# Kernel optimization log

Measured on AMD Instinct MI355X. Metric: run time of the kernel, lower is better.

## Reference

```python
import jax, jax.numpy as jnp
import numpy as np

S_CENTROIDS = 512
RADIUS = 0.5
NSAMPLE = 32
BN_EPS = 1e-5


def farthest_point_sample(xyz, s):
    # xyz: [B, N, 3] -> idx [B, s], deterministic start at index 0
    B, N, _ = xyz.shape

    def step(carry, _):
        dist, far = carry  # dist [B,N], far [B]
        centroid = jnp.take_along_axis(xyz, far[:, None, None], axis=1)  # [B,1,3]
        d = jnp.sum((xyz - centroid) ** 2, axis=-1)  # [B,N]
        dist = jnp.minimum(dist, d)
        nxt = jnp.argmax(dist, axis=-1).astype(jnp.int32)
        return (dist, nxt), far

    init = (jnp.full((B, N), 1e10, dtype=xyz.dtype), jnp.zeros((B,), jnp.int32))
    _, idx = jax.lax.scan(step, init, None, length=s)
    return idx.T  # [B, s]


def query_ball_point(radius, nsample, xyz, new_xyz):
    # xyz [B,N,3], new_xyz [B,S,3] -> group idx [B,S,nsample]
    B, N, _ = xyz.shape
    sqr = jnp.sum((new_xyz[:, :, None, :] - xyz[:, None, :, :]) ** 2, axis=-1)  # [B,S,N]
    gidx = jnp.where(sqr > radius * radius, N, jnp.arange(N, dtype=jnp.int32)[None, None, :])
    gidx = jnp.sort(gidx, axis=-1)[:, :, :nsample]  # closest-index-first valid ids
    first = gidx[:, :, :1]
    gidx = jnp.where(gidx == N, first, gidx)  # pad misses with first neighbor
    return gidx


def bn_relu(h, gamma, beta):
    # training-mode BatchNorm1d over (batch, length) dims of [BS, C, k]
    m = jnp.mean(h, axis=(0, 2), keepdims=True)
    v = jnp.var(h, axis=(0, 2), keepdims=True)
    hn = (h - m) / jnp.sqrt(v + BN_EPS)
    return jax.nn.relu(hn * gamma[None, :, None] + beta[None, :, None])


def setup_inputs() -> dict:
    key = jax.random.key(0)
    k1, k2, k3, k4 = jax.random.split(key, 4)
    B, N, Din, Dout = 16, 2048, 64, 128  # in_channels=2*Din=128
    x = jax.random.normal(k1, (B, Din, N), dtype=jnp.float32)
    coords = jax.random.uniform(k2, (B, N, 3), dtype=jnp.float32, minval=-1.0, maxval=1.0)
    W1 = jax.random.normal(k3, (Dout, 2 * Din), dtype=jnp.float32) * 0.05  # conv1 1x1 kernel
    W2 = jax.random.normal(k4, (Dout, Dout), dtype=jnp.float32) * 0.05    # conv2 1x1 kernel
    gamma1 = jnp.ones((Dout,), jnp.float32); beta1 = jnp.zeros((Dout,), jnp.float32)
    gamma2 = jnp.ones((Dout,), jnp.float32); beta2 = jnp.zeros((Dout,), jnp.float32)
    return {"x": x, "coords": coords, "W1": W1, "W2": W2,
            "gamma1": gamma1, "beta1": beta1, "gamma2": gamma2, "beta2": beta2}


def reference(x, coords, W1, W2, gamma1, beta1, gamma2, beta2):
    B = x.shape[0]
    feats = jnp.transpose(x, (0, 2, 1))  # [B, N, D]

    fidx = farthest_point_sample(coords, S_CENTROIDS)  # [B, s]
    bidx = jnp.arange(B)[:, None]
    new_xyz = coords[bidx, fidx]        # [B, s, 3]
    new_feat = feats[bidx, fidx]        # [B, s, D]

    gidx = query_ball_point(RADIUS, NSAMPLE, coords, new_xyz)  # [B, s, k]
    grouped = feats[jnp.arange(B)[:, None, None], gidx]        # [B, s, k, D]

    center = new_feat[:, :, None, :]
    agg = jnp.concatenate([grouped - center,
                           jnp.broadcast_to(center, grouped.shape)], axis=-1)  # [B, s, k, 2D]

    b, s, k, d = agg.shape
    h = jnp.transpose(agg, (0, 1, 3, 2)).reshape(b * s, d, k)  # [BS, 2D, k]
    h = bn_relu(jnp.einsum('bck,oc->bok', h, W1), gamma1, beta1)
    h = bn_relu(jnp.einsum('bck,oc->bok', h, W2), gamma2, beta2)
    pooled = jnp.max(h, axis=-1)                  # [BS, out]
    new_feature = jnp.transpose(pooled.reshape(b, s, -1), (0, 2, 1))  # [B, out, s]
    return new_xyz, new_feature
```

## Files before the change

kernel.cpp:

```cpp
#include <hip/hip_runtime.h>
#include <cstdint>

typedef unsigned int uint;
typedef unsigned short ushort_t;
typedef unsigned long long ull;
typedef __attribute__((ext_vector_type(8))) short bf16x8;
typedef __attribute__((ext_vector_type(4))) float f32x4;
typedef __attribute__((ext_vector_type(2))) float f32x2;

#define B_   16
#define N_   2048
#define S_   512
#define G_   8192
#define DIN  64
#define DOUT 128
#define K_   32
#define ATS  136

__device__ __forceinline__ uint bf16b(float f) {
  uint u = __float_as_uint(f);
  return (u + 0x7fffu + ((u >> 16) & 1u)) >> 16;
}
__device__ __forceinline__ float bf2f(uint b) { return __uint_as_float(b << 16); }

template<int CTRL, int RM>
__device__ __forceinline__ float dpp_fmax_step(float x) {
  float y = __uint_as_float((uint)__builtin_amdgcn_update_dpp(
      (int)__float_as_uint(x), (int)__float_as_uint(x), CTRL, RM, 0xf, true));
  return fmaxf(x, y);
}

__global__ __launch_bounds__(256) void fps_kernel(const float* __restrict__ coords,
                                                  int* __restrict__ fidx,
                                                  float* __restrict__ out_xyz) {
  int b = blockIdx.x;
  const float* cb = coords + (size_t)b * (N_ * 3);
  __shared__ float sptx[N_], spty[N_], sptz[N_];
  __shared__ ull   skey[2][4];
  __shared__ int   sfar[S_];
  int tid = threadIdx.x, lane = tid & 63, wid = tid >> 6;
  for (int j = tid; j < N_; j += 256) {
    sptx[j] = cb[3 * j]; spty[j] = cb[3 * j + 1]; sptz[j] = cb[3 * j + 2];
  }
  f32x2 px[4], py[4], pz[4], dist[4];
  int j0 = tid * 8;
#pragma unroll
  for (int p = 0; p < 4; ++p) {
    int j = j0 + 2 * p;
    px[p].x = cb[3 * j];     py[p].x = cb[3 * j + 1]; pz[p].x = cb[3 * j + 2];
    px[p].y = cb[3 * j + 3]; py[p].y = cb[3 * j + 4]; pz[p].y = cb[3 * j + 5];
    dist[p].x = 1e10f; dist[p].y = 1e10f;
  }
  float cx = cb[0], cy = cb[1], cz = cb[2];
  uint far = 0;
  __syncthreads();
  for (int s = 0; s < S_; ++s) {
    if (tid == 0) sfar[s] = (int)far;
    f32x2 c2x = {cx, cx}, c2y = {cy, cy}, c2z = {cz, cz};
    float bestv = -1.f; uint bestloc = 0;
#pragma unroll
    for (int p = 0; p < 4; ++p) {
      f32x2 dx, dy, dz, qx, qy, qz, s1, s2;
      asm("v_pk_add_f32 %0, %1, %2 neg_lo:[0,1] neg_hi:[0,1]" : "=v"(dx) : "v"(px[p]), "v"(c2x));
      asm("v_pk_add_f32 %0, %1, %2 neg_lo:[0,1] neg_hi:[0,1]" : "=v"(dy) : "v"(py[p]), "v"(c2y));
      asm("v_pk_add_f32 %0, %1, %2 neg_lo:[0,1] neg_hi:[0,1]" : "=v"(dz) : "v"(pz[p]), "v"(c2z));
      asm("v_pk_mul_f32 %0, %1, %1" : "=v"(qx) : "v"(dx));
      asm("v_pk_mul_f32 %0, %1, %1" : "=v"(qy) : "v"(dy));
      asm("v_pk_mul_f32 %0, %1, %1" : "=v"(qz) : "v"(dz));
      asm("v_pk_add_f32 %0, %1, %2" : "=v"(s1) : "v"(qx), "v"(qy));
      asm("v_pk_add_f32 %0, %1, %2" : "=v"(s2) : "v"(s1), "v"(qz));
      float n0 = fminf(dist[p].x, s2.x);
      float n1 = fminf(dist[p].y, s2.y);
      dist[p].x = n0; dist[p].y = n1;
      bool g0 = n0 > bestv; bestv = g0 ? n0 : bestv; bestloc = g0 ? (uint)(2 * p) : bestloc;
      bool g1 = n1 > bestv; bestv = g1 ? n1 : bestv; bestloc = g1 ? (uint)(2 * p + 1) : bestloc;
    }
    float m = bestv;
    m = dpp_fmax_step<0x111, 0xf>(m);
    m = dpp_fmax_step<0x112, 0xf>(m);
    m = dpp_fmax_step<0x114, 0xf>(m);
    m = dpp_fmax_step<0x118, 0xf>(m);
    m = dpp_fmax_step<0x142, 0xa>(m);
    m = dpp_fmax_step<0x143, 0xc>(m);
    float wmax = __uint_as_float((uint)__builtin_amdgcn_readlane((int)__float_as_uint(m), 63));
    ull mask = __ballot(bestv == wmax);
    int wl = __ffsll((long long)mask) - 1;
    uint loc = (uint)__builtin_amdgcn_readlane((int)bestloc, wl);
    uint jg = (uint)(((wid << 6) + wl) * 8) + loc;
    int pb = s & 1;
    if (lane == 0) skey[pb][wid] = ((ull)__float_as_uint(wmax) << 32) | (ull)(~jg);
    __syncthreads();
    ull k0 = skey[pb][0], k1 = skey[pb][1], k2 = skey[pb][2], k3 = skey[pb][3];
    uint w0 = ~(uint)k0, w1 = ~(uint)k1, w2 = ~(uint)k2, w3 = ~(uint)k3;
    float x0 = sptx[w0], y0 = spty[w0], z0 = sptz[w0];
    float x1 = sptx[w1], y1 = spty[w1], z1 = sptz[w1];
    float x2 = sptx[w2], y2 = spty[w2], z2 = sptz[w2];
    float x3 = sptx[w3], y3 = spty[w3], z3 = sptz[w3];
    bool t01 = k0 > k1, t23 = k2 > k3;
    ull ka = t01 ? k0 : k1;  float xa = t01 ? x0 : x1, ya = t01 ? y0 : y1, za = t01 ? z0 : z1;
    ull kb = t23 ? k2 : k3;  float xb = t23 ? x2 : x3, yb = t23 ? y2 : y3, zb = t23 ? z2 : z3;
    bool tw = ka > kb;
    far = ~(uint)(tw ? ka : kb);
    cx = tw ? xa : xb; cy = tw ? ya : yb; cz = tw ? za : zb;
  }
  __syncthreads();
  for (int s2 = tid; s2 < S_; s2 += 256) {
    int f = sfar[s2];
    fidx[b * S_ + s2] = f;
    int o = (b * S_ + s2) * 3;
    out_xyz[o] = sptx[f]; out_xyz[o + 1] = spty[f]; out_xyz[o + 2] = sptz[f];
  }
}

__global__ __launch_bounds__(256) void txp_kernel(const float* __restrict__ x,
                                                  ushort_t* __restrict__ xT) {
  __shared__ float tile[64][65];
  int b = blockIdx.x >> 5;
  int n0 = (blockIdx.x & 31) * 64;
  int nn = threadIdx.x & 63, c4 = threadIdx.x >> 6;
  const float* xb = x + (size_t)b * (DIN * N_);
#pragma unroll
  for (int i = 0; i < 16; ++i) {
    int c = c4 * 16 + i;
    tile[nn][c] = xb[(size_t)c * N_ + n0 + nn];
  }
  __syncthreads();
#pragma unroll
  for (int i = 0; i < 16; ++i) {
    int n = c4 * 16 + i;
    xT[((size_t)b * N_ + n0 + n) * 64 + nn] = (ushort_t)bf16b(tile[n][nn]);
  }
}

__global__ __launch_bounds__(256) void prep_kernel(const float* __restrict__ W1,
                                                   const float* __restrict__ W2,
                                                   ushort_t* __restrict__ Bp1,
                                                   ushort_t* __restrict__ Bpd,
                                                   ushort_t* __restrict__ Bp2) {
  int i = blockIdx.x * 256 + threadIdx.x;
  int j2 = i & 7, l = (i >> 3) & 63;
  {
    int kc = (i >> 9) & 3, nt = i >> 11;
    int o2 = nt * 16 + (l & 15);
    int c2 = kc * 32 + ((l >> 4) * 8) + j2;
    Bp2[i] = (ushort_t)bf16b(W2[o2 * 128 + c2]);
  }
  if (i < 8192) {
    int kc = (i >> 9) & 1, nt = (i >> 10) & 7;
    int o2 = nt * 16 + (l & 15);
    int c2 = kc * 32 + ((l >> 4) * 8) + j2;
    float wa = W1[o2 * 128 + c2];
    float wb = W1[o2 * 128 + 64 + c2];
    Bp1[i] = (ushort_t)bf16b(wa);
    Bpd[i] = (ushort_t)bf16b(wb - wa);
  }
}

__global__ __launch_bounds__(256) void gemm1_kernel(const ushort_t* __restrict__ xT,
    const float* __restrict__ coords, const int* __restrict__ fidx,
    const ushort_t* __restrict__ Bp1, const ushort_t* __restrict__ Bpd,
    ushort_t* __restrict__ h1T, float* __restrict__ psum, float* __restrict__ psq) {
  __shared__ int sgidx[4][K_];
  int tid = threadIdx.x;
  int lane = tid & 63, wid = tid >> 6;
  int g = __builtin_amdgcn_readfirstlane(blockIdx.x * 4 + wid);
  int b = g >> 9;
  const float* cb = coords + (size_t)b * (N_ * 3);
  int nf = fidx[g];
  {
    float cx = cb[3 * nf], cy = cb[3 * nf + 1], cz = cb[3 * nf + 2];
    int cnt = 0, first = 0;
    bool hasfirst = false;
    for (int base = 0; base < N_; base += 64) {
      int j = base + lane;
      float dx = __fsub_rn(cb[3 * j], cx);
      float dy = __fsub_rn(cb[3 * j + 1], cy);
      float dz = __fsub_rn(cb[3 * j + 2], cz);
      float d = __fadd_rn(__fadd_rn(__fmul_rn(dx, dx), __fmul_rn(dy, dy)), __fmul_rn(dz, dz));
      bool in = (d <= 0.25f);
      ull m = __ballot(in);
      if (in) {
        int pos = cnt + __popcll(m & ((1ull << lane) - 1ull));
        if (pos < K_) sgidx[wid][pos] = j;
      }
      if (!hasfirst && m) { first = base + (__ffsll((long long)m) - 1); hasfirst = true; }
      cnt += __popcll(m);
      if (cnt >= K_) break;
    }
    if (cnt < K_) {
      for (int p = cnt + lane; p < K_; p += 64) sgidx[wid][p] = first;
    }
  }
  int l15 = lane & 15, r8 = (lane >> 4) * 8;
  const ushort_t* xb64 = xT + (size_t)b * N_ * 64;
  f32x4 acc[2][8];
#pragma unroll
  for (int nt = 0; nt < 8; ++nt) acc[0][nt] = (f32x4){0.f, 0.f, 0.f, 0.f};
#pragma unroll
  for (int kc = 0; kc < 2; ++kc) {
    bf16x8 cu = *(const bf16x8*)(xb64 + nf * 64 + kc * 32 + r8);
#pragma unroll
    for (int nt = 0; nt < 8; ++nt) {
      bf16x8 bf = *(const bf16x8*)(Bpd + ((nt * 2 + kc) * 64 + lane) * 8);
      acc[0][nt] = __builtin_amdgcn_mfma_f32_16x16x32_bf16(cu, bf, acc[0][nt], 0, 0, 0);
    }
  }
#pragma unroll
  for (int nt = 0; nt < 8; ++nt) acc[1][nt] = acc[0][nt];
  int gi0 = sgidx[wid][l15];
  int gi1 = sgidx[wid][16 + l15];
#pragma unroll
  for (int kc = 0; kc < 2; ++kc) {
    bf16x8 af0 = *(const bf16x8*)(xb64 + (size_t)gi0 * 64 + kc * 32 + r8);
    bf16x8 af1 = *(const bf16x8*)(xb64 + (size_t)gi1 * 64 + kc * 32 + r8);
#pragma unroll
    for (int nt = 0; nt < 8; ++nt) {
      bf16x8 bf = *(const bf16x8*)(Bp1 + ((nt * 2 + kc) * 64 + lane) * 8);
      acc[0][nt] = __builtin_amdgcn_mfma_f32_16x16x32_bf16(af0, bf, acc[0][nt], 0, 0, 0);
      acc[1][nt] = __builtin_amdgcn_mfma_f32_16x16x32_bf16(af1, bf, acc[1][nt], 0, 0, 0);
    }
  }
#pragma unroll
  for (int nt = 0; nt < 8; ++nt) {
    float s = 0.f, q = 0.f;
#pragma unroll
    for (int mt = 0; mt < 2; ++mt)
#pragma unroll
      for (int r = 0; r < 4; ++r) { float a = acc[mt][nt][r]; s += a; q = fmaf(a, a, q); }
    s += __shfl_xor(s, 16, 64); s += __shfl_xor(s, 32, 64);
    q += __shfl_xor(q, 16, 64); q += __shfl_xor(q, 32, 64);
    if (lane < 16) {
      int o = nt * 16 + lane;
      psum[o * G_ + g] = s; psq[o * G_ + g] = q;
    }
  }
#pragma unroll
  for (int mt = 0; mt < 2; ++mt)
#pragma unroll
    for (int r = 0; r < 4; ++r) {
      int k = mt * 16 + (lane >> 4) * 4 + r;
      ushort_t* dst = h1T + (size_t)g * 4096 + k * 128 + l15;
#pragma unroll
      for (int nt = 0; nt < 8; ++nt)
        dst[nt * 16] = (ushort_t)bf16b(acc[mt][nt][r]);
    }
}

__global__ __launch_bounds__(256) void bn_finalize(const float* __restrict__ psum,
    const float* __restrict__ psq, const float* __restrict__ gamma,
    const float* __restrict__ beta, float* __restrict__ bnp) {
  int o = blockIdx.x, tid = threadIdx.x;
  double s = 0.0, q = 0.0;
  for (int g = tid; g < G_; g += 256) { s += (double)psum[o * G_ + g]; q += (double)psq[o * G_ + g]; }
  __shared__ double ss[256], qq[256];
  ss[tid] = s; qq[tid] = q; __syncthreads();
  for (int off = 128; off > 0; off >>= 1) {
    if (tid < off) { ss[tid] += ss[tid + off]; qq[tid] += qq[tid + off]; }
    __syncthreads();
  }
  if (tid == 0) {
    double n = 262144.0;
    double mean = ss[0] / n, var = qq[0] / n - mean * mean;
    float scv = (float)((double)gamma[o] / sqrt(var + 1e-5));
    bnp[2 * o] = scv;
    bnp[2 * o + 1] = (float)((double)beta[o] - mean * (double)scv);
  }
}

__global__ __launch_bounds__(256) void gemm2_kernel(const ushort_t* __restrict__ h1T,
    const ushort_t* __restrict__ Bp2, const float* __restrict__ bnp1,
    float* __restrict__ psum, float* __restrict__ psq,
    float* __restrict__ hmax, float* __restrict__ hmin) {
  __shared__ ushort_t actT[4][32 * ATS];
  int tid = threadIdx.x;
  int lane = tid & 63, wid = tid >> 6;
  int g = __builtin_amdgcn_readfirstlane(blockIdx.x * 4 + wid);
  ushort_t* aw = actT[wid];
  int c0 = (lane & 15) * 8;
  float s1[8], t1[8];
#pragma unroll
  for (int jj = 0; jj < 8; ++jj) { s1[jj] = bnp1[2 * (c0 + jj)]; t1[jj] = bnp1[2 * (c0 + jj) + 1]; }
  const uint4* src = (const uint4*)(h1T + (size_t)g * 4096);
#pragma unroll
  for (int t = 0; t < 8; ++t) {
    int idx = t * 64 + lane;
    uint4 v = src[idx];
    int k = idx >> 4;
    uint w[4] = {v.x, v.y, v.z, v.w};
    uint o4[4];
#pragma unroll
    for (int p2 = 0; p2 < 4; ++p2) {
      float a0 = fmaxf(fmaf(bf2f(w[p2] & 0xffffu), s1[2 * p2], t1[2 * p2]), 0.f);
      float a1 = fmaxf(fmaf(bf2f(w[p2] >> 16), s1[2 * p2 + 1], t1[2 * p2 + 1]), 0.f);
      o4[p2] = (bf16b(a1) << 16) | bf16b(a0);
    }
    *(uint4*)(aw + k * ATS + c0) = make_uint4(o4[0], o4[1], o4[2], o4[3]);
  }
  __syncthreads();
  f32x4 acc[2][8];
#pragma unroll
  for (int mt = 0; mt < 2; ++mt)
#pragma unroll
    for (int nt = 0; nt < 8; ++nt) acc[mt][nt] = (f32x4){0.f, 0.f, 0.f, 0.f};
#pragma unroll
  for (int kc = 0; kc < 4; ++kc) {
    bf16x8 afrag[2];
#pragma unroll
    for (int mt = 0; mt < 2; ++mt)
      afrag[mt] = *(const bf16x8*)(aw + (mt * 16 + (lane & 15)) * ATS + kc * 32 + (lane >> 4) * 8);
#pragma unroll
    for (int nt = 0; nt < 8; ++nt) {
      bf16x8 bfrag = *(const bf16x8*)(Bp2 + ((nt * 4 + kc) * 64 + lane) * 8);
      acc[0][nt] = __builtin_amdgcn_mfma_f32_16x16x32_bf16(afrag[0], bfrag, acc[0][nt], 0, 0, 0);
      acc[1][nt] = __builtin_amdgcn_mfma_f32_16x16x32_bf16(afrag[1], bfrag, acc[1][nt], 0, 0, 0);
    }
  }
#pragma unroll
  for (int nt = 0; nt < 8; ++nt) {
    float s = 0.f, q = 0.f, mx = -1e30f, mn = 1e30f;
#pragma unroll
    for (int mt = 0; mt < 2; ++mt)
#pragma unroll
      for (int r = 0; r < 4; ++r) {
        float a = acc[mt][nt][r];
        s += a; q = fmaf(a, a, q); mx = fmaxf(mx, a); mn = fminf(mn, a);
      }
    s += __shfl_xor(s, 16, 64); s += __shfl_xor(s, 32, 64);
    q += __shfl_xor(q, 16, 64); q += __shfl_xor(q, 32, 64);
    mx = fmaxf(mx, __shfl_xor(mx, 16, 64)); mx = fmaxf(mx, __shfl_xor(mx, 32, 64));
    mn = fminf(mn, __shfl_xor(mn, 16, 64)); mn = fminf(mn, __shfl_xor(mn, 32, 64));
    if (lane < 16) {
      int o = nt * 16 + lane;
      psum[o * G_ + g] = s; psq[o * G_ + g] = q;
      hmax[o * G_ + g] = mx; hmin[o * G_ + g] = mn;
    }
  }
}

__global__ __launch_bounds__(256) void pool_kernel(const float* __restrict__ hmax,
    const float* __restrict__ hmin, const float* __restrict__ bnp2,
    float* __restrict__ out) {
  int i = blockIdx.x * 256 + threadIdx.x;
  int s = i & 511;
  int o = (i >> 9) & 127;
  int b = i >> 16;
  int g = b * 512 + s;
  float scv = bnp2[2 * o], tf = bnp2[2 * o + 1];
  float v = (scv >= 0.f) ? hmax[o * G_ + g] : hmin[o * G_ + g];
  out[i] = fmaxf(fmaf(scv, v, tf), 0.f);
}

extern "C" void kernel_launch(void* const* d_in, const int* in_sizes, int n_in,
                              void* d_out, int out_size, void* d_ws, size_t ws_size,
                              hipStream_t stream) {
  const float* x      = (const float*)d_in[0];
  const float* coords = (const float*)d_in[1];
  const float* W1     = (const float*)d_in[2];
  const float* W2     = (const float*)d_in[3];
  const float* gamma1 = (const float*)d_in[4];
  const float* beta1  = (const float*)d_in[5];
  const float* gamma2 = (const float*)d_in[6];
  const float* beta2  = (const float*)d_in[7];
  float* out = (float*)d_out;
  char* ws = (char*)d_ws;
  ushort_t* h1T  = (ushort_t*)(ws);
  float* psum1 = (float*)(ws + 67108864);
  float* psq1  = (float*)(ws + 71303168);
  float* psum2 = (float*)(ws + 75497472);
  float* psq2  = (float*)(ws + 79691776);
  ushort_t* xT = (ushort_t*)(ws + 75497472);
  float* hmax  = (float*)(ws + 83886080);
  float* hmin  = (float*)(ws + 88080384);
  ushort_t* Bp1 = (ushort_t*)(ws + 92274688);
  ushort_t* Bpd = (ushort_t*)(ws + 92291072);
  ushort_t* Bp2 = (ushort_t*)(ws + 92307456);
  float* bnp1  = (float*)(ws + 92340224);
  float* bnp2  = (float*)(ws + 92341248);
  int* fidx    = (int*)(ws + 92342272);

  txp_kernel<<<512, 256, 0, stream>>>(x, xT);
  prep_kernel<<<64, 256, 0, stream>>>(W1, W2, Bp1, Bpd, Bp2);
  fps_kernel<<<16, 256, 0, stream>>>(coords, fidx, out);
  gemm1_kernel<<<2048, 256, 0, stream>>>(xT, coords, fidx, Bp1, Bpd, h1T, psum1, psq1);
  bn_finalize<<<128, 256, 0, stream>>>(psum1, psq1, gamma1, beta1, bnp1);
  gemm2_kernel<<<2048, 256, 0, stream>>>(h1T, Bp2, bnp1, psum2, psq2, hmax, hmin);
  bn_finalize<<<128, 256, 0, stream>>>(psum2, psq2, gamma2, beta2, bnp2);
  pool_kernel<<<4096, 256, 0, stream>>>(hmax, hmin, bnp2, out + 24576);
}
```

Before: 354.9 us.

## Recompute first GEMM inside second GEMM and merge front kernels into one launch

Drops the large bf16 h1 intermediate buffer. gemm1 now only computes BN statistics and stores the neighbour indices, and gemm2 recomputes the first 1x1 conv from the transposed features before applying BN1 and the second conv. The FPS, transpose and weight-prep kernels are merged into one launch so they can overlap and launch overhead shrinks. The cost is redundant GEMM1 compute and gathers in gemm2, in exchange for removing the write and re-read of a roughly 64MB intermediate.

```diff
diff --git a/kernel.cpp b/kernel.cpp
--- a/kernel.cpp
+++ b/kernel.cpp
@@ -30,136 +30,135 @@
   return fmaxf(x, y);
 }
 
-__global__ __launch_bounds__(256) void fps_kernel(const float* __restrict__ coords,
-                                                  int* __restrict__ fidx,
-                                                  float* __restrict__ out_xyz) {
-  int b = blockIdx.x;
-  const float* cb = coords + (size_t)b * (N_ * 3);
-  __shared__ float sptx[N_], spty[N_], sptz[N_];
-  __shared__ ull   skey[2][4];
-  __shared__ int   sfar[S_];
-  int tid = threadIdx.x, lane = tid & 63, wid = tid >> 6;
-  for (int j = tid; j < N_; j += 256) {
-    sptx[j] = cb[3 * j]; spty[j] = cb[3 * j + 1]; sptz[j] = cb[3 * j + 2];
-  }
-  f32x2 px[4], py[4], pz[4], dist[4];
-  int j0 = tid * 8;
-#pragma unroll
-  for (int p = 0; p < 4; ++p) {
-    int j = j0 + 2 * p;
-    px[p].x = cb[3 * j];     py[p].x = cb[3 * j + 1]; pz[p].x = cb[3 * j + 2];
-    px[p].y = cb[3 * j + 3]; py[p].y = cb[3 * j + 4]; pz[p].y = cb[3 * j + 5];
-    dist[p].x = 1e10f; dist[p].y = 1e10f;
-  }
-  float cx = cb[0], cy = cb[1], cz = cb[2];
-  uint far = 0;
-  __syncthreads();
-  for (int s = 0; s < S_; ++s) {
-    if (tid == 0) sfar[s] = (int)far;
-    f32x2 c2x = {cx, cx}, c2y = {cy, cy}, c2z = {cz, cz};
-    float bestv = -1.f; uint bestloc = 0;
+__global__ __launch_bounds__(256) void front_kernel(const float* __restrict__ coords,
+    const float* __restrict__ x, const float* __restrict__ W1,
+    const float* __restrict__ W2, int* __restrict__ fidx,
+    float* __restrict__ out_xyz, ushort_t* __restrict__ xT,
+    ushort_t* __restrict__ Bp1, ushort_t* __restrict__ Bpd,
+    ushort_t* __restrict__ Bp2) {
+  int blk = blockIdx.x;
+  int tid = threadIdx.x;
+  if (blk < 16) {
+    int b = blk;
+    const float* cb = coords + (size_t)b * (N_ * 3);
+    __shared__ float sptx[N_], spty[N_], sptz[N_];
+    __shared__ ull   skey[2][4];
+    __shared__ int   sfar[S_];
+    int lane = tid & 63, wid = tid >> 6;
+    for (int j = tid; j < N_; j += 256) {
+      sptx[j] = cb[3 * j]; spty[j] = cb[3 * j + 1]; sptz[j] = cb[3 * j + 2];
+    }
+    f32x2 px[4], py[4], pz[4], dist[4];
+    int j0 = tid * 8;
 #pragma unroll
     for (int p = 0; p < 4; ++p) {
-      f32x2 dx, dy, dz, qx, qy, qz, s1, s2;
-      asm("v_pk_add_f32 %0, %1, %2 neg_lo:[0,1] neg_hi:[0,1]" : "=v"(dx) : "v"(px[p]), "v"(c2x));
-      asm("v_pk_add_f32 %0, %1, %2 neg_lo:[0,1] neg_hi:[0,1]" : "=v"(dy) : "v"(py[p]), "v"(c2y));
-      asm("v_pk_add_f32 %0, %1, %2 neg_lo:[0,1] neg_hi:[0,1]" : "=v"(dz) : "v"(pz[p]), "v"(c2z));
-      asm("v_pk_mul_f32 %0, %1, %1" : "=v"(qx) : "v"(dx));
-      asm("v_pk_mul_f32 %0, %1, %1" : "=v"(qy) : "v"(dy));
-      asm("v_pk_mul_f32 %0, %1, %1" : "=v"(qz) : "v"(dz));
-      asm("v_pk_add_f32 %0, %1, %2" : "=v"(s1) : "v"(qx), "v"(qy));
-      asm("v_pk_add_f32 %0, %1, %2" : "=v"(s2) : "v"(s1), "v"(qz));
-      float n0 = fminf(dist[p].x, s2.x);
-      float n1 = fminf(dist[p].y, s2.y);
-      dist[p].x = n0; dist[p].y = n1;
-      bool g0 = n0 > bestv; bestv = g0 ? n0 : bestv; bestloc = g0 ? (uint)(2 * p) : bestloc;
-      bool g1 = n1 > bestv; bestv = g1 ? n1 : bestv; bestloc = g1 ? (uint)(2 * p + 1) : bestloc;
-    }
-    float m = bestv;
-    m = dpp_fmax_step<0x111, 0xf>(m);
-    m = dpp_fmax_step<0x112, 0xf>(m);
-    m = dpp_fmax_step<0x114, 0xf>(m);
-    m = dpp_fmax_step<0x118, 0xf>(m);
-    m = dpp_fmax_step<0x142, 0xa>(m);
-    m = dpp_fmax_step<0x143, 0xc>(m);
-    float wmax = __uint_as_float((uint)__builtin_amdgcn_readlane((int)__float_as_uint(m), 63));
-    ull mask = __ballot(bestv == wmax);
-    int wl = __ffsll((long long)mask) - 1;
-    uint loc = (uint)__builtin_amdgcn_readlane((int)bestloc, wl);
-    uint jg = (uint)(((wid << 6) + wl) * 8) + loc;
-    int pb = s & 1;
-    if (lane == 0) skey[pb][wid] = ((ull)__float_as_uint(wmax) << 32) | (ull)(~jg);
+      int j = j0 + 2 * p;
+      px[p].x = cb[3 * j];     py[p].x = cb[3 * j + 1]; pz[p].x = cb[3 * j + 2];
+      px[p].y = cb[3 * j + 3]; py[p].y = cb[3 * j + 4]; pz[p].y = cb[3 * j + 5];
+      dist[p].x = 1e10f; dist[p].y = 1e10f;
+    }
+    float cx = cb[0], cy = cb[1], cz = cb[2];
+    uint far = 0;
     __syncthreads();
-    ull k0 = skey[pb][0], k1 = skey[pb][1], k2 = skey[pb][2], k3 = skey[pb][3];
-    uint w0 = ~(uint)k0, w1 = ~(uint)k1, w2 = ~(uint)k2, w3 = ~(uint)k3;
-    float x0 = sptx[w0], y0 = spty[w0], z0 = sptz[w0];
-    float x1 = sptx[w1], y1 = spty[w1], z1 = sptz[w1];
-    float x2 = sptx[w2], y2 = spty[w2], z2 = sptz[w2];
-    float x3 = sptx[w3], y3 = spty[w3], z3 = sptz[w3];
-    bool t01 = k0 > k1, t23 = k2 > k3;
-    ull ka = t01 ? k0 : k1;  float xa = t01 ? x0 : x1, ya = t01 ? y0 : y1, za = t01 ? z0 : z1;
-    ull kb = t23 ? k2 : k3;  float xb = t23 ? x2 : x3, yb = t23 ? y2 : y3, zb = t23 ? z2 : z3;
-    bool tw = ka > kb;
-    far = ~(uint)(tw ? ka : kb);
-    cx = tw ? xa : xb; cy = tw ? ya : yb; cz = tw ? za : zb;
-  }
-  __syncthreads();
-  for (int s2 = tid; s2 < S_; s2 += 256) {
-    int f = sfar[s2];
-    fidx[b * S_ + s2] = f;
-    int o = (b * S_ + s2) * 3;
-    out_xyz[o] = sptx[f]; out_xyz[o + 1] = spty[f]; out_xyz[o + 2] = sptz[f];
-  }
-}
-
-__global__ __launch_bounds__(256) void txp_kernel(const float* __restrict__ x,
-                                                  ushort_t* __restrict__ xT) {
-  __shared__ float tile[64][65];
-  int b = blockIdx.x >> 5;
-  int n0 = (blockIdx.x & 31) * 64;
-  int nn = threadIdx.x & 63, c4 = threadIdx.x >> 6;
-  const float* xb = x + (size_t)b * (DIN * N_);
-#pragma unroll
-  for (int i = 0; i < 16; ++i) {
-    int c = c4 * 16 + i;
-    tile[nn][c] = xb[(size_t)c * N_ + n0 + nn];
-  }
-  __syncthreads();
-#pragma unroll
-  for (int i = 0; i < 16; ++i) {
-    int n = c4 * 16 + i;
-    xT[((size_t)b * N_ + n0 + n) * 64 + nn] = (ushort_t)bf16b(tile[n][nn]);
-  }
-}
-
-__global__ __launch_bounds__(256) void prep_kernel(const float* __restrict__ W1,
-                                                   const float* __restrict__ W2,
-                                                   ushort_t* __restrict__ Bp1,
-                                                   ushort_t* __restrict__ Bpd,
-                                                   ushort_t* __restrict__ Bp2) {
-  int i = blockIdx.x * 256 + threadIdx.x;
-  int j2 = i & 7, l = (i >> 3) & 63;
-  {
-    int kc = (i >> 9) & 3, nt = i >> 11;
-    int o2 = nt * 16 + (l & 15);
-    int c2 = kc * 32 + ((l >> 4) * 8) + j2;
-    Bp2[i] = (ushort_t)bf16b(W2[o2 * 128 + c2]);
-  }
-  if (i < 8192) {
-    int kc = (i >> 9) & 1, nt = (i >> 10) & 7;
-    int o2 = nt * 16 + (l & 15);
-    int c2 = kc * 32 + ((l >> 4) * 8) + j2;
-    float wa = W1[o2 * 128 + c2];
-    float wb = W1[o2 * 128 + 64 + c2];
-    Bp1[i] = (ushort_t)bf16b(wa);
-    Bpd[i] = (ushort_t)bf16b(wb - wa);
+    for (int s = 0; s < S_; ++s) {
+      if (tid == 0) sfar[s] = (int)far;
+      f32x2 c2x = {cx, cx}, c2y = {cy, cy}, c2z = {cz, cz};
+      float bestv = -1.f; uint bestloc = 0;
+#pragma unroll
+      for (int p = 0; p < 4; ++p) {
+        f32x2 dx, dy, dz, qx, qy, qz, s1, s2;
+        asm("v_pk_add_f32 %0, %1, %2 neg_lo:[0,1] neg_hi:[0,1]" : "=v"(dx) : "v"(px[p]), "v"(c2x));
+        asm("v_pk_add_f32 %0, %1, %2 neg_lo:[0,1] neg_hi:[0,1]" : "=v"(dy) : "v"(py[p]), "v"(c2y));
+        asm("v_pk_add_f32 %0, %1, %2 neg_lo:[0,1] neg_hi:[0,1]" : "=v"(dz) : "v"(pz[p]), "v"(c2z));
+        asm("v_pk_mul_f32 %0, %1, %1" : "=v"(qx) : "v"(dx));
+        asm("v_pk_mul_f32 %0, %1, %1" : "=v"(qy) : "v"(dy));
+        asm("v_pk_mul_f32 %0, %1, %1" : "=v"(qz) : "v"(dz));
+        asm("v_pk_add_f32 %0, %1, %2" : "=v"(s1) : "v"(qx), "v"(qy));
+        asm("v_pk_add_f32 %0, %1, %2" : "=v"(s2) : "v"(s1), "v"(qz));
+        float n0 = fminf(dist[p].x, s2.x);
+        float n1 = fminf(dist[p].y, s2.y);
+        dist[p].x = n0; dist[p].y = n1;
+        bool g0 = n0 > bestv; bestv = g0 ? n0 : bestv; bestloc = g0 ? (uint)(2 * p) : bestloc;
+        bool g1 = n1 > bestv; bestv = g1 ? n1 : bestv; bestloc = g1 ? (uint)(2 * p + 1) : bestloc;
+      }
+      float m = bestv;
+      m = dpp_fmax_step<0x111, 0xf>(m);
+      m = dpp_fmax_step<0x112, 0xf>(m);
+      m = dpp_fmax_step<0x114, 0xf>(m);
+      m = dpp_fmax_step<0x118, 0xf>(m);
+      m = dpp_fmax_step<0x142, 0xa>(m);
+      m = dpp_fmax_step<0x143, 0xc>(m);
+      float wmax = __uint_as_float((uint)__builtin_amdgcn_readlane((int)__float_as_uint(m), 63));
+      ull mask = __ballot(bestv == wmax);
+      int wl = __ffsll((long long)mask) - 1;
+      uint loc = (uint)__builtin_amdgcn_readlane((int)bestloc, wl);
+      uint jg = (uint)(((wid << 6) + wl) * 8) + loc;
+      int pb = s & 1;
+      if (lane == 0) skey[pb][wid] = ((ull)__float_as_uint(wmax) << 32) | (ull)(~jg);
+      __syncthreads();
+      ull k0 = skey[pb][0], k1 = skey[pb][1], k2 = skey[pb][2], k3 = skey[pb][3];
+      uint w0 = ~(uint)k0, w1 = ~(uint)k1, w2 = ~(uint)k2, w3 = ~(uint)k3;
+      float x0 = sptx[w0], y0 = spty[w0], z0 = sptz[w0];
+      float x1 = sptx[w1], y1 = spty[w1], z1 = sptz[w1];
+      float x2 = sptx[w2], y2 = spty[w2], z2 = sptz[w2];
+      float x3 = sptx[w3], y3 = spty[w3], z3 = sptz[w3];
+      bool t01 = k0 > k1, t23 = k2 > k3;
+      ull ka = t01 ? k0 : k1;  float xa = t01 ? x0 : x1, ya = t01 ? y0 : y1, za = t01 ? z0 : z1;
+      ull kb = t23 ? k2 : k3;  float xb = t23 ? x2 : x3, yb = t23 ? y2 : y3, zb = t23 ? z2 : z3;
+      bool tw = ka > kb;
+      far = ~(uint)(tw ? ka : kb);
+      cx = tw ? xa : xb; cy = tw ? ya : yb; cz = tw ? za : zb;
+    }
+    __syncthreads();
+    for (int s2 = tid; s2 < S_; s2 += 256) {
+      int f = sfar[s2];
+      fidx[b * S_ + s2] = f;
+      int o = (b * S_ + s2) * 3;
+      out_xyz[o] = sptx[f]; out_xyz[o + 1] = spty[f]; out_xyz[o + 2] = sptz[f];
+    }
+  } else if (blk < 528) {
+    __shared__ float tile[64][65];
+    int blk2 = blk - 16;
+    int b = blk2 >> 5;
+    int n0 = (blk2 & 31) * 64;
+    int nn = tid & 63, c4 = tid >> 6;
+    const float* xb = x + (size_t)b * (DIN * N_);
+#pragma unroll
+    for (int i = 0; i < 16; ++i) {
+      int c = c4 * 16 + i;
+      tile[nn][c] = xb[(size_t)c * N_ + n0 + nn];
+    }
+    __syncthreads();
+#pragma unroll
+    for (int i = 0; i < 16; ++i) {
+      int n = c4 * 16 + i;
+      xT[((size_t)b * N_ + n0 + n) * 64 + nn] = (ushort_t)bf16b(tile[n][nn]);
+    }
+  } else {
+    int i = (blk - 528) * 256 + tid;
+    int j2 = i & 7, l = (i >> 3) & 63;
+    {
+      int kc = (i >> 9) & 3, nt = i >> 11;
+      int o2 = nt * 16 + (l & 15);
+      int c2 = kc * 32 + ((l >> 4) * 8) + j2;
+      Bp2[i] = (ushort_t)bf16b(W2[o2 * 128 + c2]);
+    }
+    if (i < 8192) {
+      int kc = (i >> 9) & 1, nt = (i >> 10) & 7;
+      int o2 = nt * 16 + (l & 15);
+      int c2 = kc * 32 + ((l >> 4) * 8) + j2;
+      float wa = W1[o2 * 128 + c2];
+      float wb = W1[o2 * 128 + 64 + c2];
+      Bp1[i] = (ushort_t)bf16b(wa);
+      Bpd[i] = (ushort_t)bf16b(wb - wa);
+    }
   }
 }
 
 __global__ __launch_bounds__(256) void gemm1_kernel(const ushort_t* __restrict__ xT,
     const float* __restrict__ coords, const int* __restrict__ fidx,
     const ushort_t* __restrict__ Bp1, const ushort_t* __restrict__ Bpd,
-    ushort_t* __restrict__ h1T, float* __restrict__ psum, float* __restrict__ psq) {
+    int* __restrict__ gidx, float* __restrict__ psum, float* __restrict__ psq) {
   __shared__ int sgidx[4][K_];
   int tid = threadIdx.x;
   int lane = tid & 63, wid = tid >> 6;
@@ -191,6 +190,7 @@
       for (int p = cnt + lane; p < K_; p += 64) sgidx[wid][p] = first;
     }
   }
+  if (lane < K_) gidx[g * K_ + lane] = sgidx[wid][lane];
   int l15 = lane & 15, r8 = (lane >> 4) * 8;
   const ushort_t* xb64 = xT + (size_t)b * N_ * 64;
   f32x4 acc[2][8];
@@ -234,16 +234,6 @@
       psum[o * G_ + g] = s; psq[o * G_ + g] = q;
     }
   }
-#pragma unroll
-  for (int mt = 0; mt < 2; ++mt)
-#pragma unroll
-    for (int r = 0; r < 4; ++r) {
-      int k = mt * 16 + (lane >> 4) * 4 + r;
-      ushort_t* dst = h1T + (size_t)g * 4096 + k * 128 + l15;
-#pragma unroll
-      for (int nt = 0; nt < 8; ++nt)
-        dst[nt * 16] = (ushort_t)bf16b(acc[mt][nt][r]);
-    }
 }
 
 __global__ __launch_bounds__(256) void bn_finalize(const float* __restrict__ psum,
@@ -267,7 +257,9 @@
   }
 }
 
-__global__ __launch_bounds__(256) void gemm2_kernel(const ushort_t* __restrict__ h1T,
+__global__ __launch_bounds__(256) void gemm2_kernel(const ushort_t* __restrict__ xT,
+    const int* __restrict__ fidx, const int* __restrict__ gidx,
+    const ushort_t* __restrict__ Bp1, const ushort_t* __restrict__ Bpd,
     const ushort_t* __restrict__ Bp2, const float* __restrict__ bnp1,
     float* __restrict__ psum, float* __restrict__ psq,
     float* __restrict__ hmax, float* __restrict__ hmin) {
@@ -275,44 +267,71 @@
   int tid = threadIdx.x;
   int lane = tid & 63, wid = tid >> 6;
   int g = __builtin_amdgcn_readfirstlane(blockIdx.x * 4 + wid);
+  int b = g >> 9;
+  int l15 = lane & 15, r8 = (lane >> 4) * 8;
+  const ushort_t* xb64 = xT + (size_t)b * N_ * 64;
+  int nf = fidx[g];
+  f32x4 acc[2][8];
+#pragma unroll
+  for (int nt = 0; nt < 8; ++nt) acc[0][nt] = (f32x4){0.f, 0.f, 0.f, 0.f};
+#pragma unroll
+  for (int kc = 0; kc < 2; ++kc) {
+    bf16x8 cu = *(const bf16x8*)(xb64 + nf * 64 + kc * 32 + r8);
+#pragma unroll
+    for (int nt = 0; nt < 8; ++nt) {
+      bf16x8 bf = *(const bf16x8*)(Bpd + ((nt * 2 + kc) * 64 + lane) * 8);
+      acc[0][nt] = __builtin_amdgcn_mfma_f32_16x16x32_bf16(cu, bf, acc[0][nt], 0, 0, 0);
+    }
+  }
+#pragma unroll
+  for (int nt = 0; nt < 8; ++nt) acc[1][nt] = acc[0][nt];
+  int gi0 = gidx[g * K_ + l15];
+  int gi1 = gidx[g * K_ + 16 + l15];
+#pragma unroll
+  for (int kc = 0; kc < 2; ++kc) {
+    bf16x8 af0 = *(const bf16x8*)(xb64 + (size_t)gi0 * 64 + kc * 32 + r8);
+    bf16x8 af1 = *(const bf16x8*)(xb64 + (size_t)gi1 * 64 + kc * 32 + r8);
+#pragma unroll
+    for (int nt = 0; nt < 8; ++nt) {
+      bf16x8 bf = *(const bf16x8*)(Bp1 + ((nt * 2 + kc) * 64 + lane) * 8);
+      acc[0][nt] = __builtin_amdgcn_mfma_f32_16x16x32_bf16(af0, bf, acc[0][nt], 0, 0, 0);
+      acc[1][nt] = __builtin_amdgcn_mfma_f32_16x16x32_bf16(af1, bf, acc[1][nt], 0, 0, 0);
+    }
+  }
+  float s1v[8], t1v[8];
+#pragma unroll
+  for (int nt = 0; nt < 8; ++nt) {
+    int o = nt * 16 + l15;
+    s1v[nt] = bnp1[2 * o]; t1v[nt] = bnp1[2 * o + 1];
+  }
   ushort_t* aw = actT[wid];
-  int c0 = (lane & 15) * 8;
-  float s1[8], t1[8];
-#pragma unroll
-  for (int jj = 0; jj < 8; ++jj) { s1[jj] = bnp1[2 * (c0 + jj)]; t1[jj] = bnp1[2 * (c0 + jj) + 1]; }
-  const uint4* src = (const uint4*)(h1T + (size_t)g * 4096);
-#pragma unroll
-  for (int t = 0; t < 8; ++t) {
-    int idx = t * 64 + lane;
-    uint4 v = src[idx];
-    int k = idx >> 4;
-    uint w[4] = {v.x, v.y, v.z, v.w};
-    uint o4[4];
-#pragma unroll
-    for (int p2 = 0; p2 < 4; ++p2) {
-      float a0 = fmaxf(fmaf(bf2f(w[p2] & 0xffffu), s1[2 * p2], t1[2 * p2]), 0.f);
-      float a1 = fmaxf(fmaf(bf2f(w[p2] >> 16), s1[2 * p2 + 1], t1[2 * p2 + 1]), 0.f);
-      o4[p2] = (bf16b(a1) << 16) | bf16b(a0);
-    }
-    *(uint4*)(aw + k * ATS + c0) = make_uint4(o4[0], o4[1], o4[2], o4[3]);
-  }
-  __syncthreads();
-  f32x4 acc[2][8];
 #pragma unroll
   for (int mt = 0; mt < 2; ++mt)
 #pragma unroll
-    for (int nt = 0; nt < 8; ++nt) acc[mt][nt] = (f32x4){0.f, 0.f, 0.f, 0.f};
+    for (int r = 0; r < 4; ++r) {
+      int k = mt * 16 + (lane >> 4) * 4 + r;
+#pragma unroll
+      for (int nt = 0; nt < 8; ++nt) {
+        float a = fmaxf(fmaf(acc[mt][nt][r], s1v[nt], t1v[nt]), 0.f);
+        aw[k * ATS + nt * 16 + l15] = (ushort_t)bf16b(a);
+      }
+    }
+  f32x4 acc2[2][8];
+#pragma unroll
+  for (int mt = 0; mt < 2; ++mt)
+#pragma unroll
+    for (int nt = 0; nt < 8; ++nt) acc2[mt][nt] = (f32x4){0.f, 0.f, 0.f, 0.f};
 #pragma unroll
   for (int kc = 0; kc < 4; ++kc) {
     bf16x8 afrag[2];
 #pragma unroll
     for (int mt = 0; mt < 2; ++mt)
-      afrag[mt] = *(const bf16x8*)(aw + (mt * 16 + (lane & 15)) * ATS + kc * 32 + (lane >> 4) * 8);
+      afrag[mt] = *(const bf16x8*)(aw + (mt * 16 + l15) * ATS + kc * 32 + r8);
 #pragma unroll
     for (int nt = 0; nt < 8; ++nt) {
       bf16x8 bfrag = *(const bf16x8*)(Bp2 + ((nt * 4 + kc) * 64 + lane) * 8);
-      acc[0][nt] = __builtin_amdgcn_mfma_f32_16x16x32_bf16(afrag[0], bfrag, acc[0][nt], 0, 0, 0);
-      acc[1][nt] = __builtin_amdgcn_mfma_f32_16x16x32_bf16(afrag[1], bfrag, acc[1][nt], 0, 0, 0);
+      acc2[0][nt] = __builtin_amdgcn_mfma_f32_16x16x32_bf16(afrag[0], bfrag, acc2[0][nt], 0, 0, 0);
+      acc2[1][nt] = __builtin_amdgcn_mfma_f32_16x16x32_bf16(afrag[1], bfrag, acc2[1][nt], 0, 0, 0);
     }
   }
 #pragma unroll
@@ -322,7 +341,7 @@
     for (int mt = 0; mt < 2; ++mt)
 #pragma unroll
       for (int r = 0; r < 4; ++r) {
-        float a = acc[mt][nt][r];
+        float a = acc2[mt][nt][r];
         s += a; q = fmaf(a, a, q); mx = fmaxf(mx, a); mn = fminf(mn, a);
       }
     s += __shfl_xor(s, 16, 64); s += __shfl_xor(s, 32, 64);
@@ -363,27 +382,26 @@
   const float* beta2  = (const float*)d_in[7];
   float* out = (float*)d_out;
   char* ws = (char*)d_ws;
-  ushort_t* h1T  = (ushort_t*)(ws);
-  float* psum1 = (float*)(ws + 67108864);
-  float* psq1  = (float*)(ws + 71303168);
-  float* psum2 = (float*)(ws + 75497472);
-  float* psq2  = (float*)(ws + 79691776);
-  ushort_t* xT = (ushort_t*)(ws + 75497472);
-  float* hmax  = (float*)(ws + 83886080);
-  float* hmin  = (float*)(ws + 88080384);
-  ushort_t* Bp1 = (ushort_t*)(ws + 92274688);
-  ushort_t* Bpd = (ushort_t*)(ws + 92291072);
-  ushort_t* Bp2 = (ushort_t*)(ws + 92307456);
-  float* bnp1  = (float*)(ws + 92340224);
-  float* bnp2  = (float*)(ws + 92341248);
-  int* fidx    = (int*)(ws + 92342272);
-
-  txp_kernel<<<512, 256, 0, stream>>>(x, xT);
-  prep_kernel<<<64, 256, 0, stream>>>(W1, W2, Bp1, Bpd, Bp2);
-  fps_kernel<<<16, 256, 0, stream>>>(coords, fidx, out);
-  gemm1_kernel<<<2048, 256, 0, stream>>>(xT, coords, fidx, Bp1, Bpd, h1T, psum1, psq1);
+  float* psum1 = (float*)(ws);
+  float* psq1  = (float*)(ws + 4194304);
+  float* psum2 = (float*)(ws + 8388608);
+  float* psq2  = (float*)(ws + 12582912);
+  float* hmax  = (float*)(ws + 16777216);
+  float* hmin  = (float*)(ws + 20971520);
+  ushort_t* xT = (ushort_t*)(ws + 25165824);
+  ushort_t* Bp1 = (ushort_t*)(ws + 29360128);
+  ushort_t* Bpd = (ushort_t*)(ws + 29376512);
+  ushort_t* Bp2 = (ushort_t*)(ws + 29392896);
+  float* bnp1  = (float*)(ws + 29425664);
+  float* bnp2  = (float*)(ws + 29426688);
+  int* fidx    = (int*)(ws + 29427712);
+  int* gidx    = (int*)(ws + 29460480);
+
+  front_kernel<<<592, 256, 0, stream>>>(coords, x, W1, W2, fidx, out, xT, Bp1, Bpd, Bp2);
+  gemm1_kernel<<<2048, 256, 0, stream>>>(xT, coords, fidx, Bp1, Bpd, gidx, psum1, psq1);
   bn_finalize<<<128, 256, 0, stream>>>(psum1, psq1, gamma1, beta1, bnp1);
-  gemm2_kernel<<<2048, 256, 0, stream>>>(h1T, Bp2, bnp1, psum2, psq2, hmax, hmin);
+  gemm2_kernel<<<2048, 256, 0, stream>>>(xT, fidx, gidx, Bp1, Bpd, Bp2, bnp1,
+                                         psum2, psq2, hmax, hmin);
   bn_finalize<<<128, 256, 0, stream>>>(psum2, psq2, gamma2, beta2, bnp2);
   pool_kernel<<<4096, 256, 0, stream>>>(hmax, hmin, bnp2, out + 24576);
 }
```

Result: faster. 347.2 us (-2.2%).
